# Kernel optimization log

Measured on AMD Instinct MI355X. Metric: run time of the kernel, lower is better.

Reference implementation:

```python
import jax, jax.numpy as jnp
import numpy as np

ALPHA = 300.0  # attractor strength (exp variant: exp(-alpha*|dx|^gamma)*dx, gamma=2)


def setup_inputs() -> dict:
    key = jax.random.key(0)
    k0, k1, k2, k3 = jax.random.split(key, 4)
    n, c, h, w = 4, 256, 128, 128
    mlp_dim, n_attractors, n_bins = 128, 16, 64
    x = jax.random.normal(k0, (n, c, h, w), jnp.float32)
    b_prev = jax.random.uniform(k1, (n, n_bins, h, w), jnp.float32)  # bin centers
    w1 = jax.random.normal(k2, (mlp_dim, c), jnp.float32) * 0.02
    b1 = jnp.zeros((mlp_dim,), jnp.float32)
    w2 = jax.random.normal(k3, (n_attractors, mlp_dim), jnp.float32) * 0.02
    b2 = jnp.zeros((n_attractors,), jnp.float32)
    return {"x": x, "b_prev": b_prev, "w1": w1, "b1": b1, "w2": w2, "b2": b2}


def reference(x, b_prev, w1, b1, w2, b2):
    # 1x1 conv MLP head: Conv2d(c->mlp) -> ReLU -> Conv2d(mlp->n_attractors) -> Softplus
    hfeat = jax.nn.relu(jnp.einsum('nchw,oc->nohw', x, w1) + b1[None, :, None, None])
    A = jax.nn.softplus(jnp.einsum('nchw,oc->nohw', hfeat, w2) + b2[None, :, None, None])
    # b_prev interpolated to (h, w) == identity here (same spatial size)
    b_centers = b_prev
    # dx: [n, n_attractors, n_bins, h, w]
    dx = A[:, :, None, :, :] - b_centers[:, None, :, :, :]
    # exp attractor with gamma=2: exp(-alpha*dx^2) * dx, summed over attractors ('sum' kind)
    delta_c = jnp.sum(jnp.exp(-ALPHA * dx * dx) * dx, axis=1)
    b_new_centers = b_centers + delta_c
    return (b_new_centers, b_new_centers)
```

## Files before the change

### kernel.cpp

```cpp
#include <hip/hip_runtime.h>
#include <hip/hip_bf16.h>
#include <stdint.h>


#define HW 16384
#define ALPHA 300.0f

typedef short bf16x8_t __attribute__((ext_vector_type(8)));
typedef float f32x4_t __attribute__((ext_vector_type(4)));
typedef unsigned int u32x4_t __attribute__((ext_vector_type(4)));

__device__ __forceinline__ unsigned short f2bf(float f) {
  unsigned int u = __builtin_bit_cast(unsigned int, f);
  u += 0x7fffu + ((u >> 16) & 1u);
  return (unsigned short)(u >> 16);
}
__device__ __forceinline__ unsigned int pack2(float a, float b) {
  return (unsigned int)f2bf(a) | ((unsigned int)f2bf(b) << 16);
}

__global__ void zoed_prep(const float* __restrict__ w1,
                          const float* __restrict__ w2,
                          unsigned short* __restrict__ blob) {
  int i = blockIdx.x * 256 + threadIdx.x;
  if (i < 32768) {
    int o = i >> 8, c = i & 255;
    float v = w1[i];
    int idx = (c >> 5) * 4096 + o * 32 + ((((c >> 3) & 3) ^ (o & 3)) << 3) + (c & 7);
    blob[idx] = f2bf(v);
  } else {
    int i2 = i - 32768;
    int a = i2 >> 7, o = i2 & 127;
    float v = w2[i2];
    int idx = 32768 + (o >> 5) * 512 + a * 32 + ((((o >> 3) & 3) ^ (a & 3)) << 3) + (o & 7);
    blob[idx] = f2bf(v);
  }
}

__global__ __launch_bounds__(256, 2) void zoed_fused(
    const float* __restrict__ x, const float* __restrict__ bprev,
    const float* __restrict__ b1, const float* __restrict__ b2,
    const unsigned short* __restrict__ wblob, float* __restrict__ out) {
  __shared__ __align__(16) char smem[45056];
  char* xbuf = smem;
  char* w1buf = smem + 8192;
  char* hid = smem;
  char* Albuf = smem + 32768;
  char* w2buf = smem + 40960;

  const int t = threadIdx.x;
  const int lane = t & 63;
  const int l15 = lane & 15;
  const int quad = lane >> 4;
  const int wv = t >> 6;
  const int wm = wv & 1;
  const int wn = wv >> 1;
  const int sw = ((quad ^ (lane & 3)) << 4);

  const int blk = blockIdx.x;
  const int n = blk >> 7;
  const int p0 = (blk & 127) << 7;

  *(u32x4_t*)(w2buf + t * 16) =
      *(const u32x4_t*)((const char*)wblob + 65536 + t * 16);

  f32x4_t acc[4][4];
#pragma unroll
  for (int i = 0; i < 4; i++)
#pragma unroll
    for (int j = 0; j < 4; j++) acc[i][j] = (f32x4_t){0.f, 0.f, 0.f, 0.f};

  const int sp = t & 127;
  const int sg = t >> 7;

  for (int kb = 0; kb < 8; ++kb) {
    __syncthreads();
#pragma unroll
    for (int gi = 0; gi < 2; ++gi) {
      int g = sg + gi * 2;
      const float* xs = x + (size_t)(n * 256 + kb * 32 + g * 8) * HW + p0 + sp;
      float f0 = xs[0 * HW], f1 = xs[1 * HW], f2 = xs[2 * HW], f3 = xs[3 * HW];
      float f4 = xs[4 * HW], f5 = xs[5 * HW], f6 = xs[6 * HW], f7 = xs[7 * HW];
      u32x4_t v = {pack2(f0, f1), pack2(f2, f3), pack2(f4, f5), pack2(f6, f7)};
      *(u32x4_t*)(xbuf + sp * 64 + ((g ^ (sp & 3)) << 4)) = v;
    }
    {
      const char* src = (const char*)wblob + kb * 8192 + t * 32;
      *(u32x4_t*)(w1buf + t * 32) = *(const u32x4_t*)src;
      *(u32x4_t*)(w1buf + t * 32 + 16) = *(const u32x4_t*)(src + 16);
    }
    __syncthreads();
    bf16x8_t af[4], bfm[4];
#pragma unroll
    for (int tm = 0; tm < 4; tm++)
      af[tm] = *(const bf16x8_t*)(w1buf + (wm * 64 + tm * 16 + l15) * 64 + sw);
#pragma unroll
    for (int tn = 0; tn < 4; tn++)
      bfm[tn] = *(const bf16x8_t*)(xbuf + (wn * 64 + tn * 16 + l15) * 64 + sw);
#pragma unroll
    for (int tm = 0; tm < 4; tm++)
#pragma unroll
      for (int tn = 0; tn < 4; tn++)
        acc[tm][tn] = __builtin_amdgcn_mfma_f32_16x16x32_bf16(
            af[tm], bfm[tn], acc[tm][tn], 0, 0, 0);
  }

  __syncthreads();
#pragma unroll
  for (int tm = 0; tm < 4; tm++) {
    f32x4_t b1v = *(const f32x4_t*)(b1 + wm * 64 + tm * 16 + quad * 4);
    int kc = wm * 2 + (tm >> 1);
    int g = (tm & 1) * 2 + (quad >> 1);
    int off8 = (quad & 1) * 8;
#pragma unroll
    for (int tn = 0; tn < 4; tn++) {
      f32x4_t h = acc[tm][tn] + b1v;
      h[0] = fmaxf(h[0], 0.f);
      h[1] = fmaxf(h[1], 0.f);
      h[2] = fmaxf(h[2], 0.f);
      h[3] = fmaxf(h[3], 0.f);
      int prow = wn * 64 + tn * 16 + l15;
      unsigned int* dst = (unsigned int*)(hid + kc * 8192 + prow * 64 +
                                          ((g ^ (prow & 3)) << 4) + off8);
      dst[0] = pack2(h[0], h[1]);
      dst[1] = pack2(h[2], h[3]);
    }
  }
  __syncthreads();
  bf16x8_t a2[4];
#pragma unroll
  for (int kc = 0; kc < 4; kc++)
    a2[kc] = *(const bf16x8_t*)(w2buf + kc * 1024 + l15 * 64 + sw);
  f32x4_t acc2[2];
  acc2[0] = (f32x4_t){0.f, 0.f, 0.f, 0.f};
  acc2[1] = (f32x4_t){0.f, 0.f, 0.f, 0.f};
#pragma unroll
  for (int tn = 0; tn < 2; tn++) {
    int prow = wv * 32 + tn * 16 + l15;
#pragma unroll
    for (int kc = 0; kc < 4; kc++) {
      bf16x8_t bh = *(const bf16x8_t*)(hid + kc * 8192 + prow * 64 + sw);
      acc2[tn] = __builtin_amdgcn_mfma_f32_16x16x32_bf16(a2[kc], bh, acc2[tn],
                                                         0, 0, 0);
    }
  }
  f32x4_t b2v = *(const f32x4_t*)(b2 + quad * 4);
#pragma unroll
  for (int tn = 0; tn < 2; tn++) {
    f32x4_t z = acc2[tn] + b2v;
    f32x4_t spv;
#pragma unroll
    for (int r = 0; r < 4; r++) {
      float zz = z[r];
      spv[r] = fmaxf(zz, 0.f) + log1pf(__expf(-fabsf(zz)));
    }
    int prow = wv * 32 + tn * 16 + l15;
    *(f32x4_t*)(Albuf + prow * 64 + ((quad ^ (prow & 3)) << 4)) = spv;
  }
  __syncthreads();
  {
    const int p = t & 127;
    const int half = t >> 7;
    float Av[16];
#pragma unroll
    for (int q = 0; q < 4; q++) {
      f32x4_t v = *(const f32x4_t*)(Albuf + p * 64 + ((q ^ (p & 3)) << 4));
      Av[q * 4 + 0] = v[0];
      Av[q * 4 + 1] = v[1];
      Av[q * 4 + 2] = v[2];
      Av[q * 4 + 3] = v[3];
    }
    size_t base = (size_t)n * 64 * HW + (size_t)(half * 32) * HW + (size_t)(p0 + p);
    const float* bp = bprev + base;
    float* o1 = out + base;
    float* o2 = out + (size_t)4 * 64 * HW + base;
#pragma unroll 4
    for (int b = 0; b < 32; b++) {
      float c = bp[(size_t)b * HW];
      float d0 = 0.f, d1 = 0.f;
#pragma unroll
      for (int a = 0; a < 8; a++) {
        float dx = Av[a] - c;
        float e = __expf(dx * dx * -ALPHA);
        d0 = fmaf(e, dx, d0);
      }
#pragma unroll
      for (int a = 8; a < 16; a++) {
        float dx = Av[a] - c;
        float e = __expf(dx * dx * -ALPHA);
        d1 = fmaf(e, dx, d1);
      }
      float r = c + (d0 + d1);
      __builtin_nontemporal_store(r, o1 + (size_t)b * HW);
      __builtin_nontemporal_store(r, o2 + (size_t)b * HW);
    }
  }
}

extern "C" void kernel_launch(void* const* d_in, const int* in_sizes, int n_in,
                              void* d_out, int out_size, void* d_ws,
                              size_t ws_size, hipStream_t stream) {
  const float* x = (const float*)d_in[0];
  const float* bprev = (const float*)d_in[1];
  const float* w1 = (const float*)d_in[2];
  const float* b1 = (const float*)d_in[3];
  const float* w2 = (const float*)d_in[4];
  const float* b2 = (const float*)d_in[5];
  float* outp = (float*)d_out;
  unsigned short* blob = (unsigned short*)d_ws;

  zoed_prep<<<136, 256, 0, stream>>>(w1, w2, blob);
  zoed_fused<<<512, 256, 0, stream>>>(x, bprev, b1, b2, blob, outp);
}
```

Before: 140.1 us.

## Halve pixel tile per block and register-prefetch next K chunk

Each block now covers 64 pixels instead of 128, which doubles the grid to 1024 blocks and roughly halves shared memory, and launch bounds are raised to allow four blocks per CU. The x and w1 loads for the next K chunk are issued into registers before the current chunk's MFMAs, so global latency can overlap compute. The second GEMM and the attractor stage are rebalanced to 16 bins per wave group. The cost is that w1 is reloaded from memory by twice as many blocks, and the tighter register budget could cause spills.

```diff
diff --git a/kernel.cpp b/kernel.cpp
--- a/kernel.cpp
+++ b/kernel.cpp
@@ -37,16 +37,16 @@
   }
 }
 
-__global__ __launch_bounds__(256, 2) void zoed_fused(
+__global__ __launch_bounds__(256, 4) void zoed_fused(
     const float* __restrict__ x, const float* __restrict__ bprev,
     const float* __restrict__ b1, const float* __restrict__ b2,
     const unsigned short* __restrict__ wblob, float* __restrict__ out) {
-  __shared__ __align__(16) char smem[45056];
+  __shared__ __align__(16) char smem[24576];
   char* xbuf = smem;
-  char* w1buf = smem + 8192;
+  char* w1buf = smem + 4096;
   char* hid = smem;
-  char* Albuf = smem + 32768;
-  char* w2buf = smem + 40960;
+  char* Albuf = smem + 16384;
+  char* w2buf = smem + 20480;
 
   const int t = threadIdx.x;
   const int lane = t & 63;
@@ -58,49 +58,62 @@
   const int sw = ((quad ^ (lane & 3)) << 4);
 
   const int blk = blockIdx.x;
-  const int n = blk >> 7;
-  const int p0 = (blk & 127) << 7;
+  const int n = blk >> 8;
+  const int p0 = (blk & 255) << 6;
 
   *(u32x4_t*)(w2buf + t * 16) =
       *(const u32x4_t*)((const char*)wblob + 65536 + t * 16);
 
-  f32x4_t acc[4][4];
+  f32x4_t acc[4][2];
 #pragma unroll
   for (int i = 0; i < 4; i++)
 #pragma unroll
-    for (int j = 0; j < 4; j++) acc[i][j] = (f32x4_t){0.f, 0.f, 0.f, 0.f};
-
-  const int sp = t & 127;
-  const int sg = t >> 7;
+    for (int j = 0; j < 2; j++) acc[i][j] = (f32x4_t){0.f, 0.f, 0.f, 0.f};
+
+  const int sp = t & 63;
+  const int sg = t >> 6;
+
+  const float* xsbase = x + (size_t)(n * 256 + sg * 8) * HW + p0 + sp;
+  float xf0, xf1, xf2, xf3, xf4, xf5, xf6, xf7;
+  u32x4_t wfa, wfb;
+  {
+    const float* xs = xsbase;
+    xf0 = xs[0 * HW]; xf1 = xs[1 * HW]; xf2 = xs[2 * HW]; xf3 = xs[3 * HW];
+    xf4 = xs[4 * HW]; xf5 = xs[5 * HW]; xf6 = xs[6 * HW]; xf7 = xs[7 * HW];
+    const char* wsrc = (const char*)wblob + t * 32;
+    wfa = *(const u32x4_t*)wsrc;
+    wfb = *(const u32x4_t*)(wsrc + 16);
+  }
 
   for (int kb = 0; kb < 8; ++kb) {
     __syncthreads();
-#pragma unroll
-    for (int gi = 0; gi < 2; ++gi) {
-      int g = sg + gi * 2;
-      const float* xs = x + (size_t)(n * 256 + kb * 32 + g * 8) * HW + p0 + sp;
-      float f0 = xs[0 * HW], f1 = xs[1 * HW], f2 = xs[2 * HW], f3 = xs[3 * HW];
-      float f4 = xs[4 * HW], f5 = xs[5 * HW], f6 = xs[6 * HW], f7 = xs[7 * HW];
-      u32x4_t v = {pack2(f0, f1), pack2(f2, f3), pack2(f4, f5), pack2(f6, f7)};
-      *(u32x4_t*)(xbuf + sp * 64 + ((g ^ (sp & 3)) << 4)) = v;
-    }
     {
-      const char* src = (const char*)wblob + kb * 8192 + t * 32;
-      *(u32x4_t*)(w1buf + t * 32) = *(const u32x4_t*)src;
-      *(u32x4_t*)(w1buf + t * 32 + 16) = *(const u32x4_t*)(src + 16);
+      u32x4_t v = {pack2(xf0, xf1), pack2(xf2, xf3), pack2(xf4, xf5),
+                   pack2(xf6, xf7)};
+      *(u32x4_t*)(xbuf + sp * 64 + ((sg ^ (sp & 3)) << 4)) = v;
+      *(u32x4_t*)(w1buf + t * 32) = wfa;
+      *(u32x4_t*)(w1buf + t * 32 + 16) = wfb;
     }
     __syncthreads();
-    bf16x8_t af[4], bfm[4];
+    if (kb < 7) {
+      const float* xs = xsbase + (size_t)((kb + 1) * 32) * HW;
+      xf0 = xs[0 * HW]; xf1 = xs[1 * HW]; xf2 = xs[2 * HW]; xf3 = xs[3 * HW];
+      xf4 = xs[4 * HW]; xf5 = xs[5 * HW]; xf6 = xs[6 * HW]; xf7 = xs[7 * HW];
+      const char* wsrc = (const char*)wblob + (kb + 1) * 8192 + t * 32;
+      wfa = *(const u32x4_t*)wsrc;
+      wfb = *(const u32x4_t*)(wsrc + 16);
+    }
+    bf16x8_t af[4], bfm[2];
 #pragma unroll
     for (int tm = 0; tm < 4; tm++)
       af[tm] = *(const bf16x8_t*)(w1buf + (wm * 64 + tm * 16 + l15) * 64 + sw);
 #pragma unroll
-    for (int tn = 0; tn < 4; tn++)
-      bfm[tn] = *(const bf16x8_t*)(xbuf + (wn * 64 + tn * 16 + l15) * 64 + sw);
+    for (int tn = 0; tn < 2; tn++)
+      bfm[tn] = *(const bf16x8_t*)(xbuf + (wn * 32 + tn * 16 + l15) * 64 + sw);
 #pragma unroll
     for (int tm = 0; tm < 4; tm++)
 #pragma unroll
-      for (int tn = 0; tn < 4; tn++)
+      for (int tn = 0; tn < 2; tn++)
         acc[tm][tn] = __builtin_amdgcn_mfma_f32_16x16x32_bf16(
             af[tm], bfm[tn], acc[tm][tn], 0, 0, 0);
   }
@@ -113,54 +126,43 @@
     int g = (tm & 1) * 2 + (quad >> 1);
     int off8 = (quad & 1) * 8;
 #pragma unroll
-    for (int tn = 0; tn < 4; tn++) {
+    for (int tn = 0; tn < 2; tn++) {
       f32x4_t h = acc[tm][tn] + b1v;
       h[0] = fmaxf(h[0], 0.f);
       h[1] = fmaxf(h[1], 0.f);
       h[2] = fmaxf(h[2], 0.f);
       h[3] = fmaxf(h[3], 0.f);
-      int prow = wn * 64 + tn * 16 + l15;
-      unsigned int* dst = (unsigned int*)(hid + kc * 8192 + prow * 64 +
+      int prow = wn * 32 + tn * 16 + l15;
+      unsigned int* dst = (unsigned int*)(hid + kc * 4096 + prow * 64 +
                                           ((g ^ (prow & 3)) << 4) + off8);
       dst[0] = pack2(h[0], h[1]);
       dst[1] = pack2(h[2], h[3]);
     }
   }
   __syncthreads();
-  bf16x8_t a2[4];
-#pragma unroll
-  for (int kc = 0; kc < 4; kc++)
-    a2[kc] = *(const bf16x8_t*)(w2buf + kc * 1024 + l15 * 64 + sw);
-  f32x4_t acc2[2];
-  acc2[0] = (f32x4_t){0.f, 0.f, 0.f, 0.f};
-  acc2[1] = (f32x4_t){0.f, 0.f, 0.f, 0.f};
-#pragma unroll
-  for (int tn = 0; tn < 2; tn++) {
-    int prow = wv * 32 + tn * 16 + l15;
+  {
+    f32x4_t acc2 = (f32x4_t){0.f, 0.f, 0.f, 0.f};
+    const int prow = wv * 16 + l15;
 #pragma unroll
     for (int kc = 0; kc < 4; kc++) {
-      bf16x8_t bh = *(const bf16x8_t*)(hid + kc * 8192 + prow * 64 + sw);
-      acc2[tn] = __builtin_amdgcn_mfma_f32_16x16x32_bf16(a2[kc], bh, acc2[tn],
-                                                         0, 0, 0);
-    }
-  }
-  f32x4_t b2v = *(const f32x4_t*)(b2 + quad * 4);
-#pragma unroll
-  for (int tn = 0; tn < 2; tn++) {
-    f32x4_t z = acc2[tn] + b2v;
+      bf16x8_t a2 = *(const bf16x8_t*)(w2buf + kc * 1024 + l15 * 64 + sw);
+      bf16x8_t bh = *(const bf16x8_t*)(hid + kc * 4096 + prow * 64 + sw);
+      acc2 = __builtin_amdgcn_mfma_f32_16x16x32_bf16(a2, bh, acc2, 0, 0, 0);
+    }
+    f32x4_t b2v = *(const f32x4_t*)(b2 + quad * 4);
+    f32x4_t z = acc2 + b2v;
     f32x4_t spv;
 #pragma unroll
     for (int r = 0; r < 4; r++) {
       float zz = z[r];
       spv[r] = fmaxf(zz, 0.f) + log1pf(__expf(-fabsf(zz)));
     }
-    int prow = wv * 32 + tn * 16 + l15;
     *(f32x4_t*)(Albuf + prow * 64 + ((quad ^ (prow & 3)) << 4)) = spv;
   }
   __syncthreads();
   {
-    const int p = t & 127;
-    const int half = t >> 7;
+    const int p = t & 63;
+    const int grp = t >> 6;
     float Av[16];
 #pragma unroll
     for (int q = 0; q < 4; q++) {
@@ -170,12 +172,12 @@
       Av[q * 4 + 2] = v[2];
       Av[q * 4 + 3] = v[3];
     }
-    size_t base = (size_t)n * 64 * HW + (size_t)(half * 32) * HW + (size_t)(p0 + p);
+    size_t base = (size_t)n * 64 * HW + (size_t)(grp * 16) * HW + (size_t)(p0 + p);
     const float* bp = bprev + base;
     float* o1 = out + base;
     float* o2 = out + (size_t)4 * 64 * HW + base;
 #pragma unroll 4
-    for (int b = 0; b < 32; b++) {
+    for (int b = 0; b < 16; b++) {
       float c = bp[(size_t)b * HW];
       float d0 = 0.f, d1 = 0.f;
 #pragma unroll
@@ -210,5 +212,5 @@
   unsigned short* blob = (unsigned short*)d_ws;
 
   zoed_prep<<<136, 256, 0, stream>>>(w1, w2, blob);
-  zoed_fused<<<512, 256, 0, stream>>>(x, bprev, b1, b2, blob, outp);
-}
+  zoed_fused<<<1024, 256, 0, stream>>>(x, bprev, b1, b2, blob, outp);
+}
```

Measured after the change: 136.8 us. 1.02x faster.
